# Performance work log

Measured on AMD Instinct MI355X. Metric: run time of the kernel, lower is better.

The kernel has to match this reference:

```python
import jax, jax.numpy as jnp
import numpy as np

N_EMBD = 512
N_HEAD = 8
HEAD_DIM = N_EMBD // N_HEAD


def setup_inputs() -> dict:
    key = jax.random.key(0)
    ks = jax.random.split(key, 10)
    B, Tx, Tc, C = 8, 1024, 2048, N_EMBD
    s = 1.0 / np.sqrt(C)
    return {
        "x": jax.random.normal(ks[0], (B, Tx, C), dtype=jnp.float32),
        "context": jax.random.normal(ks[1], (B, Tc, C), dtype=jnp.float32),
        "Wq": jax.random.normal(ks[2], (C, C), dtype=jnp.float32) * s,
        "bq": jnp.zeros((C,), dtype=jnp.float32),
        "Wk": jax.random.normal(ks[3], (C, C), dtype=jnp.float32) * s,
        "bk": jnp.zeros((C,), dtype=jnp.float32),
        "Wv": jax.random.normal(ks[4], (C, C), dtype=jnp.float32) * s,
        "bv": jnp.zeros((C,), dtype=jnp.float32),
        "Wo": jax.random.normal(ks[5], (C, C), dtype=jnp.float32) * s,
        "bo": jnp.zeros((C,), dtype=jnp.float32),
    }


def reference(x, context, Wq, bq, Wk, bk, Wv, bv, Wo, bo):
    B, Tx, C = x.shape
    Tc = context.shape[1]
    nh, hd = N_HEAD, C // N_HEAD
    # projections (torch Linear: y = x @ W.T + b)
    q = (x @ Wq.T + bq).reshape(B, Tx, nh, hd).transpose(0, 2, 1, 3)
    k = (context @ Wk.T + bk).reshape(B, Tc, nh, hd).transpose(0, 2, 1, 3)
    v = (context @ Wv.T + bv).reshape(B, Tc, nh, hd).transpose(0, 2, 1, 3)
    # attention scores (B, nh, Tx, Tc)
    att = jnp.einsum("bhqd,bhkd->bhqk", q, k) * (1.0 / np.sqrt(hd))
    att = jax.nn.softmax(att, axis=-1)
    y = jnp.einsum("bhqk,bhkd->bhqd", att, v)
    y = y.transpose(0, 2, 1, 3).reshape(B, Tx, C)
    att_mean = att.mean(axis=1)  # (B, Tx, Tc)
    y = y @ Wo.T + bo
    return (y, att_mean)
```

## Files before the change

kernel.cpp:

```cpp
#include <hip/hip_runtime.h>

#define DEVI __device__ __forceinline__

typedef short bf16x8 __attribute__((ext_vector_type(8)));
typedef short bf16x4 __attribute__((ext_vector_type(4)));
typedef float f32x4 __attribute__((ext_vector_type(4)));

constexpr int Bb = 8, TX = 1024, TC = 2048, CC = 512, NH = 8, HD = 64;
constexpr float LOG2E = 1.44269504f;

DEVI unsigned short f2bf(float f) {
  union { float f; unsigned u; } v; v.f = f;
  return (unsigned short)((v.u + 0x7FFFu + ((v.u >> 16) & 1u)) >> 16);
}

DEVI unsigned cvtpk(float lo, float hi) {
  unsigned r;
  asm("v_cvt_pk_bf16_f32 %0, %1, %2" : "=v"(r) : "v"(lo), "v"(hi));
  return r;
}

DEVI f32x4 mfma16(bf16x8 a, bf16x8 b, f32x4 c) {
  return __builtin_amdgcn_mfma_f32_16x16x32_bf16(a, b, c, 0, 0, 0);
}

DEVI f32x4 zero4() { f32x4 z = {0.f, 0.f, 0.f, 0.f}; return z; }

DEVI float max3f(float a, float b, float c) { return fmaxf(fmaxf(a, b), c); }

DEVI void gload_lds16(const unsigned short* g, unsigned short* l) {
  __builtin_amdgcn_global_load_lds(
      (const __attribute__((address_space(1))) void*)g,
      (__attribute__((address_space(3))) void*)l, 16, 0, 0);
}

__global__ __launch_bounds__(256) void cvt_bf16(
    const float* __restrict__ src, unsigned short* __restrict__ dst, int n8) {
  int i = blockIdx.x * 256 + threadIdx.x;
  const int stride = gridDim.x * 256;
  for (; i < n8; i += stride) {
    f32x4 a = *(const f32x4*)(src + (size_t)i * 8);
    f32x4 b = *(const f32x4*)(src + (size_t)i * 8 + 4);
    bf16x8 v;
#pragma unroll
    for (int j = 0; j < 4; j++) {
      v[j] = (short)f2bf(a[j]);
      v[j + 4] = (short)f2bf(b[j]);
    }
    *(bf16x8*)(dst + (size_t)i * 8) = v;
  }
}

template <int MODE>
__global__ __launch_bounds__(256, 3) void gemm128(
    const unsigned short* __restrict__ A, const unsigned short* __restrict__ W,
    const float* __restrict__ bias, void* __restrict__ outp, int tlog2, float scale) {
  __shared__ __align__(16) unsigned short As[2][128 * 32];
  __shared__ __align__(16) unsigned short Bs[2][128 * 32];

  const int tid = threadIdx.x;
  const int wid = tid >> 6, l = tid & 63, l15 = l & 15, lhi = l >> 4;
  const int wm = wid >> 1, wn = wid & 1;
  const int mbase = blockIdx.y * 128, nbase = blockIdx.x * 128;

  f32x4 acc[4][4];
#pragma unroll
  for (int i = 0; i < 4; i++)
#pragma unroll
    for (int j = 0; j < 4; j++) acc[i][j] = zero4();

  auto stage = [&](int buf, int k0) {
#pragma unroll
    for (int i = 0; i < 2; i++) {
      const int u = wid * 128 + i * 64 + l;
      const int row = u >> 2;
      const int gc = ((u & 3) ^ ((row >> 1) & 3)) * 8;
      const int lo = (wid * 128 + i * 64) * 8;
      gload_lds16(A + (size_t)(mbase + row) * CC + k0 + gc, &As[buf][lo]);
      gload_lds16(W + (size_t)(nbase + row) * CC + k0 + gc, &Bs[buf][lo]);
    }
  };

  stage(0, 0);

  const int sA = (lhi ^ ((l15 >> 1) & 3)) << 3;

  constexpr int NK = CC / 32;
  for (int kt = 0; kt < NK; kt++) {
    const int cur = kt & 1;
    __syncthreads();
    if (kt + 1 < NK) stage(cur ^ 1, (kt + 1) * 32);

    bf16x8 af[4], bfr[4];
#pragma unroll
    for (int mi = 0; mi < 4; mi++)
      af[mi] = *(const bf16x8*)&As[cur][(wm * 64 + mi * 16 + l15) * 32 + sA];
#pragma unroll
    for (int ni = 0; ni < 4; ni++)
      bfr[ni] = *(const bf16x8*)&Bs[cur][(wn * 64 + ni * 16 + l15) * 32 + sA];
#pragma unroll
    for (int mi = 0; mi < 4; mi++)
#pragma unroll
      for (int ni = 0; ni < 4; ni++)
        acc[mi][ni] = mfma16(af[mi], bfr[ni], acc[mi][ni]);
  }

#pragma unroll
  for (int mi = 0; mi < 4; mi++)
#pragma unroll
    for (int ni = 0; ni < 4; ni++)
#pragma unroll
      for (int r = 0; r < 4; r++) {
        int grow = mbase + wm * 64 + mi * 16 + 4 * lhi + r;
        int gcol = nbase + wn * 64 + ni * 16 + l15;
        float val = (acc[mi][ni][r] + bias[gcol]) * scale;
        if (MODE == 0) {
          int T = 1 << tlog2;
          int bq = grow >> tlog2, tt = grow & (T - 1);
          int h = gcol >> 6, d = gcol & 63;
          size_t oidx = ((size_t)(bq * NH + h) * T + tt) * HD + d;
          ((unsigned short*)outp)[oidx] = f2bf(val);
        } else {
          ((float*)outp)[(size_t)grow * CC + gcol] = val;
        }
      }
}

__global__ __launch_bounds__(256, 2) void kv_gemm128(
    const unsigned short* __restrict__ A, const unsigned short* __restrict__ Wk,
    const unsigned short* __restrict__ Wv, const float* __restrict__ bk,
    const float* __restrict__ bv, unsigned short* __restrict__ k_out,
    unsigned short* __restrict__ v_out) {
  __shared__ __align__(16) unsigned short As[2][128 * 32];
  __shared__ __align__(16) unsigned short Bks[2][128 * 32];
  __shared__ __align__(16) unsigned short Bvs[2][128 * 32];

  const int tid = threadIdx.x;
  const int wid = tid >> 6, l = tid & 63, l15 = l & 15, lhi = l >> 4;
  const int wm = wid >> 1, wn = wid & 1;
  const int mbase = blockIdx.y * 128, nbase = blockIdx.x * 128;

  f32x4 acck[4][4], accv[4][4];
#pragma unroll
  for (int i = 0; i < 4; i++)
#pragma unroll
    for (int j = 0; j < 4; j++) { acck[i][j] = zero4(); accv[i][j] = zero4(); }

  auto stage = [&](int buf, int k0) {
#pragma unroll
    for (int i = 0; i < 2; i++) {
      const int u = wid * 128 + i * 64 + l;
      const int row = u >> 2;
      const int gc = ((u & 3) ^ ((row >> 1) & 3)) * 8;
      const int lo = (wid * 128 + i * 64) * 8;
      gload_lds16(A + (size_t)(mbase + row) * CC + k0 + gc, &As[buf][lo]);
      gload_lds16(Wk + (size_t)(nbase + row) * CC + k0 + gc, &Bks[buf][lo]);
      gload_lds16(Wv + (size_t)(nbase + row) * CC + k0 + gc, &Bvs[buf][lo]);
    }
  };

  stage(0, 0);

  const int sA = (lhi ^ ((l15 >> 1) & 3)) << 3;

  constexpr int NK = CC / 32;
  for (int kt = 0; kt < NK; kt++) {
    const int cur = kt & 1;
    __syncthreads();
    if (kt + 1 < NK) stage(cur ^ 1, (kt + 1) * 32);

    bf16x8 af[4], kf[4], vf[4];
#pragma unroll
    for (int mi = 0; mi < 4; mi++)
      af[mi] = *(const bf16x8*)&As[cur][(wm * 64 + mi * 16 + l15) * 32 + sA];
#pragma unroll
    for (int ni = 0; ni < 4; ni++) {
      kf[ni] = *(const bf16x8*)&Bks[cur][(wn * 64 + ni * 16 + l15) * 32 + sA];
      vf[ni] = *(const bf16x8*)&Bvs[cur][(wn * 64 + ni * 16 + l15) * 32 + sA];
    }
#pragma unroll
    for (int mi = 0; mi < 4; mi++)
#pragma unroll
      for (int ni = 0; ni < 4; ni++) {
        acck[mi][ni] = mfma16(af[mi], kf[ni], acck[mi][ni]);
        accv[mi][ni] = mfma16(af[mi], vf[ni], accv[mi][ni]);
      }
  }

#pragma unroll
  for (int mi = 0; mi < 4; mi++)
#pragma unroll
    for (int ni = 0; ni < 4; ni++)
#pragma unroll
      for (int r = 0; r < 4; r++) {
        int grow = mbase + wm * 64 + mi * 16 + 4 * lhi + r;
        int gcol = nbase + wn * 64 + ni * 16 + l15;
        int bq = grow >> 11, tt = grow & (TC - 1);
        int h = gcol >> 6, d = gcol & 63;
        float kv = acck[mi][ni][r] + bk[gcol];
        float vv = accv[mi][ni][r] + bv[gcol];
        k_out[((size_t)(bq * NH + h) * TC + tt) * HD + d] = f2bf(kv);
        v_out[((size_t)(bq * NH + h) * HD + d) * TC + tt] = f2bf(vv);
      }
}

__global__ __launch_bounds__(512) void attn_fwd(
    const unsigned short* __restrict__ Qw, const unsigned short* __restrict__ Kw,
    const unsigned short* __restrict__ Vtw, unsigned short* __restrict__ y_pre,
    float* __restrict__ m_ws, float* __restrict__ il_ws) {
  __shared__ __align__(16) unsigned short ktl[2][64 * 64];
  __shared__ __align__(16) unsigned short vtl[2][64 * 64];

  const int tid = threadIdx.x;
  const int wid = tid >> 6, l = tid & 63, l15 = l & 15, lhi = l >> 4;
  const int qg = blockIdx.x, h = blockIdx.y, b = blockIdx.z;
  const int qbase = qg * 128 + wid * 16;

  const unsigned short* Qh = Qw + (size_t)(b * NH + h) * TX * HD;
  const unsigned short* Kh = Kw + (size_t)(b * NH + h) * TC * HD;
  const unsigned short* Vt = Vtw + (size_t)(b * NH + h) * TC * HD;

  bf16x8 aq0 = *(const bf16x8*)(Qh + (size_t)(qbase + l15) * HD + lhi * 8);
  bf16x8 aq1 = *(const bf16x8*)(Qh + (size_t)(qbase + l15) * HD + 32 + lhi * 8);

  bf16x8 ones;
#pragma unroll
  for (int j = 0; j < 8; j++) ones[j] = (short)0x3F80;

  f32x4 accy[4];
#pragma unroll
  for (int db = 0; db < 4; db++) accy[db] = zero4();
  f32x4 accl = zero4();
  float mrun = -1e30f;

  const int sl0 = l15 + ((lhi & 1) << 5);
  const int sl1 = sl0 + 16;
  const bool sel = ((lhi >> 1) & 1) != 0;

  const int rs0 = (lhi ^ (l15 & 7)) << 3;
  const int rs1 = ((lhi ^ 4) ^ (l15 & 7)) << 3;

  const int sr = tid >> 3;
  const int ssw = ((tid & 7) ^ (sr & 7)) << 3;
  const int sc0 = (tid & 7) * 8;

  bf16x8 kr = *(const bf16x8*)(Kh + (size_t)sr * HD + sc0);
  bf16x8 vp = *(const bf16x8*)(Vt + (size_t)sr * TC + sc0);
  *(bf16x8*)&ktl[0][sr * 64 + ssw] = kr;
  *(bf16x8*)&vtl[0][sr * 64 + ssw] = vp;
  __syncthreads();

  constexpr int NT = TC / 64;
  for (int kt = 0; kt < NT; kt++) {
    const int cur = kt & 1;

    if (kt + 1 < NT) {
      const int keyn = (kt + 1) * 64;
      kr = *(const bf16x8*)(Kh + (size_t)(keyn + sr) * HD + sc0);
      vp = *(const bf16x8*)(Vt + (size_t)sr * TC + keyn + sc0);
    }

    f32x4 s[4];
    __builtin_amdgcn_s_setprio(1);
#pragma unroll
    for (int kb = 0; kb < 4; kb++) {
      bf16x8 bk0 = *(const bf16x8*)&ktl[cur][(kb * 16 + l15) * 64 + rs0];
      bf16x8 bk1 = *(const bf16x8*)&ktl[cur][(kb * 16 + l15) * 64 + rs1];
      f32x4 a = zero4();
      a = mfma16(bk0, aq0, a);
      a = mfma16(bk1, aq1, a);
      s[kb] = a;
    }
    __builtin_amdgcn_s_setprio(0);

    float t0 = max3f(s[0][0], s[0][1], s[0][2]);
    float t1 = max3f(s[0][3], s[1][0], s[1][1]);
    float t2 = max3f(s[1][2], s[1][3], s[2][0]);
    float t3 = max3f(s[2][1], s[2][2], s[2][3]);
    float t4 = max3f(s[3][0], s[3][1], s[3][2]);
    float mx = fmaxf(max3f(t0, t1, t2), max3f(t3, t4, s[3][3]));
    mx = fmaxf(mx, __shfl_xor(mx, 16));
    mx = fmaxf(mx, __shfl_xor(mx, 32));

    if (__any(mx - mrun > 7.0f)) {
      float mn = fmaxf(mrun, mx);
      float sc = exp2f(mrun - mn);
      mrun = mn;
#pragma unroll
      for (int r = 0; r < 4; r++) accl[r] *= sc;
#pragma unroll
      for (int db = 0; db < 4; db++)
#pragma unroll
        for (int r = 0; r < 4; r++) accy[db][r] *= sc;
    }

    float p[4][4];
#pragma unroll
    for (int kb = 0; kb < 4; kb++)
#pragma unroll
      for (int r = 0; r < 4; r++) p[kb][r] = exp2f(s[kb][r] - mrun);

    unsigned pkw[4][2];
#pragma unroll
    for (int kb = 0; kb < 4; kb++) {
      pkw[kb][0] = cvtpk(p[kb][0], p[kb][1]);
      pkw[kb][1] = cvtpk(p[kb][2], p[kb][3]);
    }
    unsigned a00 = (unsigned)__shfl((int)pkw[0][0], sl0);
    unsigned a01 = (unsigned)__shfl((int)pkw[0][1], sl0);
    unsigned a10 = (unsigned)__shfl((int)pkw[1][0], sl0);
    unsigned a11 = (unsigned)__shfl((int)pkw[1][1], sl0);
    unsigned c00 = (unsigned)__shfl((int)pkw[0][0], sl1);
    unsigned c01 = (unsigned)__shfl((int)pkw[0][1], sl1);
    unsigned c10 = (unsigned)__shfl((int)pkw[1][0], sl1);
    unsigned c11 = (unsigned)__shfl((int)pkw[1][1], sl1);
    unsigned e00 = (unsigned)__shfl((int)pkw[2][0], sl0);
    unsigned e01 = (unsigned)__shfl((int)pkw[2][1], sl0);
    unsigned e10 = (unsigned)__shfl((int)pkw[3][0], sl0);
    unsigned e11 = (unsigned)__shfl((int)pkw[3][1], sl0);
    unsigned g00 = (unsigned)__shfl((int)pkw[2][0], sl1);
    unsigned g01 = (unsigned)__shfl((int)pkw[2][1], sl1);
    unsigned g10 = (unsigned)__shfl((int)pkw[3][0], sl1);
    unsigned g11 = (unsigned)__shfl((int)pkw[3][1], sl1);
    union { unsigned u[4]; bf16x8 v; } B0, B1;
    B0.u[0] = sel ? a10 : a00;
    B0.u[1] = sel ? a11 : a01;
    B0.u[2] = sel ? c10 : c00;
    B0.u[3] = sel ? c11 : c01;
    B1.u[0] = sel ? e10 : e00;
    B1.u[1] = sel ? e11 : e01;
    B1.u[2] = sel ? g10 : g00;
    B1.u[3] = sel ? g11 : g01;

    __builtin_amdgcn_s_setprio(1);
#pragma unroll
    for (int db = 0; db < 4; db++) {
      bf16x8 bv0 = *(const bf16x8*)&vtl[cur][(db * 16 + l15) * 64 + rs0];
      bf16x8 bv1 = *(const bf16x8*)&vtl[cur][(db * 16 + l15) * 64 + rs1];
      accy[db] = mfma16(bv0, B0.v, accy[db]);
      accy[db] = mfma16(bv1, B1.v, accy[db]);
    }
    accl = mfma16(ones, B0.v, accl);
    accl = mfma16(ones, B1.v, accl);
    __builtin_amdgcn_s_setprio(0);

    if (kt + 1 < NT) {
      const int nxt = cur ^ 1;
      *(bf16x8*)&ktl[nxt][sr * 64 + ssw] = kr;
      *(bf16x8*)&vtl[nxt][sr * 64 + ssw] = vp;
    }
    __syncthreads();
  }

  const float il = 1.f / accl[0];

#pragma unroll
  for (int db = 0; db < 4; db++) {
    bf16x4 o;
#pragma unroll
    for (int r = 0; r < 4; r++) o[r] = (short)f2bf(accy[db][r] * il);
    *(bf16x4*)(y_pre + (size_t)(b * TX + qbase + l15) * CC + h * HD + db * 16 +
               4 * lhi) = o;
  }
  if (lhi == 0) {
    int idx = (b * NH + h) * TX + qbase + l15;
    m_ws[idx] = mrun;
    il_ws[idx] = il;
  }
}

__global__ __launch_bounds__(512) void att_mean_k(
    const unsigned short* __restrict__ Qw, const unsigned short* __restrict__ Kw,
    const float* __restrict__ m_ws, const float* __restrict__ il_ws,
    float* __restrict__ attm) {
  __shared__ __align__(16) unsigned short ktl[2][64 * 64];

  const int tid = threadIdx.x;
  const int wid = tid >> 6, l = tid & 63, l15 = l & 15, lhi = l >> 4;
  const int qbase = blockIdx.x * 128 + wid * 16;
  const int keyb = blockIdx.y * 64;
  const int b = blockIdx.z;

  const unsigned short* Qb = Qw + (size_t)b * NH * TX * HD;
  const unsigned short* Kb = Kw + (size_t)b * NH * TC * HD;

  const int rs0 = (lhi ^ (l15 & 7)) << 3;
  const int rs1 = ((lhi ^ 4) ^ (l15 & 7)) << 3;

  const int sr = tid >> 3;
  const int ssw = ((tid & 7) ^ (sr & 7)) << 3;
  const int sc0 = (tid & 7) * 8;

  bf16x8 aq0[2], aq1[2];
  f32x4 mm[2], ii[2];

  auto load_q = [&](int h, int p) {
    const unsigned short* qp =
        Qb + ((size_t)h * TX + qbase + l15) * HD + lhi * 8;
    aq0[p] = *(const bf16x8*)qp;
    aq1[p] = *(const bf16x8*)(qp + 32);
    mm[p] = *(const f32x4*)(m_ws + (size_t)(b * NH + h) * TX + qbase + 4 * lhi);
    ii[p] = *(const f32x4*)(il_ws + (size_t)(b * NH + h) * TX + qbase + 4 * lhi);
  };

  bf16x8 kr = *(const bf16x8*)(Kb + ((size_t)keyb + sr) * HD + sc0);
  load_q(0, 0);
  *(bf16x8*)&ktl[0][sr * 64 + ssw] = kr;
  __syncthreads();

  f32x4 am[4];
#pragma unroll
  for (int kb = 0; kb < 4; kb++) am[kb] = zero4();

#pragma unroll
  for (int h = 0; h < NH; h++) {
    const int cur = h & 1;

    if (h + 1 < NH) {
      kr = *(const bf16x8*)(Kb + ((size_t)(h + 1) * TC + keyb + sr) * HD + sc0);
      load_q(h + 1, cur ^ 1);
    }

#pragma unroll
    for (int kb = 0; kb < 4; kb++) {
      bf16x8 bk0 = *(const bf16x8*)&ktl[cur][(kb * 16 + l15) * 64 + rs0];
      bf16x8 bk1 = *(const bf16x8*)&ktl[cur][(kb * 16 + l15) * 64 + rs1];
      f32x4 a = zero4();
      a = mfma16(aq0[cur], bk0, a);
      a = mfma16(aq1[cur], bk1, a);
#pragma unroll
      for (int r = 0; r < 4; r++)
        am[kb][r] += exp2f(a[r] - mm[cur][r]) * ii[cur][r];
    }

    if (h + 1 < NH) {
      const int nxt = cur ^ 1;
      *(bf16x8*)&ktl[nxt][sr * 64 + ssw] = kr;
    }
    __syncthreads();
  }

#pragma unroll
  for (int kb = 0; kb < 4; kb++)
#pragma unroll
    for (int r = 0; r < 4; r++) {
      int trow = qbase + 4 * lhi + r;
      attm[(size_t)(b * TX + trow) * TC + keyb + kb * 16 + l15] = am[kb][r] * 0.125f;
    }
}

extern "C" void kernel_launch(void* const* d_in, const int* in_sizes, int n_in,
                              void* d_out, int out_size, void* d_ws, size_t ws_size,
                              hipStream_t stream) {
  const float* x   = (const float*)d_in[0];
  const float* ctx = (const float*)d_in[1];
  const float* Wq  = (const float*)d_in[2];
  const float* bq  = (const float*)d_in[3];
  const float* Wk  = (const float*)d_in[4];
  const float* bk  = (const float*)d_in[5];
  const float* Wv  = (const float*)d_in[6];
  const float* bv  = (const float*)d_in[7];
  const float* Wo  = (const float*)d_in[8];
  const float* bo  = (const float*)d_in[9];

  float* y_out = (float*)d_out;
  float* attm  = y_out + (size_t)Bb * TX * CC;

  unsigned short* q_ws = (unsigned short*)d_ws;
  unsigned short* k_ws = q_ws + (size_t)Bb * NH * TX * HD;
  unsigned short* v_ws = k_ws + (size_t)Bb * NH * TC * HD;
  float* m_ws  = (float*)(v_ws + (size_t)Bb * NH * TC * HD);
  float* il_ws = m_ws + (size_t)Bb * NH * TX;
  unsigned short* y_pre = (unsigned short*)(il_ws + (size_t)Bb * NH * TX);
  unsigned short* wb = y_pre + (size_t)Bb * TX * CC;
  unsigned short* wbq = wb, *wbk = wb + CC * CC, *wbv = wb + 2 * CC * CC,
                 *wbo = wb + 3 * CC * CC;

  unsigned short* xb = k_ws;
  unsigned short* cb = (unsigned short*)attm;

  const int NX8 = Bb * TX * CC / 8, NC8 = Bb * TC * CC / 8, NW8 = CC * CC / 8;
  cvt_bf16<<<dim3(2048), 256, 0, stream>>>(x, xb, NX8);
  cvt_bf16<<<dim3(2048), 256, 0, stream>>>(ctx, cb, NC8);
  cvt_bf16<<<dim3(128), 256, 0, stream>>>(Wq, wbq, NW8);
  cvt_bf16<<<dim3(128), 256, 0, stream>>>(Wk, wbk, NW8);
  cvt_bf16<<<dim3(128), 256, 0, stream>>>(Wv, wbv, NW8);
  cvt_bf16<<<dim3(128), 256, 0, stream>>>(Wo, wbo, NW8);

  gemm128<0><<<dim3(CC / 128, (Bb * TX) / 128), 256, 0, stream>>>(
      xb, wbq, bq, q_ws, 10, 0.125f * LOG2E);
  kv_gemm128<<<dim3(CC / 128, (Bb * TC) / 128), 256, 0, stream>>>(
      cb, wbk, wbv, bk, bv, k_ws, v_ws);
  attn_fwd<<<dim3(TX / 128, NH, Bb), 512, 0, stream>>>(q_ws, k_ws, v_ws, y_pre, m_ws, il_ws);
  att_mean_k<<<dim3(TX / 128, TC / 64, Bb), 512, 0, stream>>>(q_ws, k_ws, m_ws, il_ws, attm);
  gemm128<1><<<dim3(CC / 128, (Bb * TX) / 128), 256, 0, stream>>>(
      y_pre, wbo, bo, y_out, 10, 1.0f);
}
```

Measured before the change: 220.7 us.

## Merge conversion kernels and preload all K heads into LDS in att_mean

The six fp32-to-bf16 conversion launches become one grid-stride kernel covering all six tensors, which removes launch gaps. In att_mean_k, all eight heads' K tiles are now loaded up front into LDS with direct global-to-LDS loads, in a single batch followed by one barrier. This replaces the per-head double-buffered register staging and its per-iteration __syncthreads, and Q, m and il prefetch is deepened to three slots. LDS per block grows to 64KB, which can limit how many blocks fit per CU despite the launch_bounds occupancy hint.

```diff
diff --git a/kernel.cpp b/kernel.cpp
--- a/kernel.cpp
+++ b/kernel.cpp
@@ -34,11 +34,9 @@
       (__attribute__((address_space(3))) void*)l, 16, 0, 0);
 }
 
-__global__ __launch_bounds__(256) void cvt_bf16(
-    const float* __restrict__ src, unsigned short* __restrict__ dst, int n8) {
-  int i = blockIdx.x * 256 + threadIdx.x;
-  const int stride = gridDim.x * 256;
-  for (; i < n8; i += stride) {
+DEVI void cvt_region(const float* __restrict__ src,
+                     unsigned short* __restrict__ dst, int n8, int i0, int stride) {
+  for (int i = i0; i < n8; i += stride) {
     f32x4 a = *(const f32x4*)(src + (size_t)i * 8);
     f32x4 b = *(const f32x4*)(src + (size_t)i * 8 + 4);
     bf16x8 v;
@@ -49,6 +47,23 @@
     }
     *(bf16x8*)(dst + (size_t)i * 8) = v;
   }
+}
+
+__global__ __launch_bounds__(256) void cvt_all(
+    const float* __restrict__ s0, unsigned short* __restrict__ d0, int n0,
+    const float* __restrict__ s1, unsigned short* __restrict__ d1, int n1,
+    const float* __restrict__ s2, unsigned short* __restrict__ d2, int n2,
+    const float* __restrict__ s3, unsigned short* __restrict__ d3, int n3,
+    const float* __restrict__ s4, unsigned short* __restrict__ d4, int n4,
+    const float* __restrict__ s5, unsigned short* __restrict__ d5, int n5) {
+  const int i0 = blockIdx.x * 256 + threadIdx.x;
+  const int stride = gridDim.x * 256;
+  cvt_region(s0, d0, n0, i0, stride);
+  cvt_region(s1, d1, n1, i0, stride);
+  cvt_region(s2, d2, n2, i0, stride);
+  cvt_region(s3, d3, n3, i0, stride);
+  cvt_region(s4, d4, n4, i0, stride);
+  cvt_region(s5, d5, n5, i0, stride);
 }
 
 template <int MODE>
@@ -369,11 +384,11 @@
   }
 }
 
-__global__ __launch_bounds__(512) void att_mean_k(
+__global__ __launch_bounds__(512, 4) void att_mean_k(
     const unsigned short* __restrict__ Qw, const unsigned short* __restrict__ Kw,
     const float* __restrict__ m_ws, const float* __restrict__ il_ws,
     float* __restrict__ attm) {
-  __shared__ __align__(16) unsigned short ktl[2][64 * 64];
+  __shared__ __align__(16) unsigned short ktl[NH][64 * 64];
 
   const int tid = threadIdx.x;
   const int wid = tid >> 6, l = tid & 63, l15 = l & 15, lhi = l >> 4;
@@ -387,12 +402,11 @@
   const int rs0 = (lhi ^ (l15 & 7)) << 3;
   const int rs1 = ((lhi ^ 4) ^ (l15 & 7)) << 3;
 
-  const int sr = tid >> 3;
-  const int ssw = ((tid & 7) ^ (sr & 7)) << 3;
-  const int sc0 = (tid & 7) * 8;
-
-  bf16x8 aq0[2], aq1[2];
-  f32x4 mm[2], ii[2];
+  const int srow = (wid * 64 + l) >> 3;
+  const int sgc = ((l & 7) ^ (srow & 7)) * 8;
+
+  bf16x8 aq0[3], aq1[3];
+  f32x4 mm[3], ii[3];
 
   auto load_q = [&](int h, int p) {
     const unsigned short* qp =
@@ -403,9 +417,12 @@
     ii[p] = *(const f32x4*)(il_ws + (size_t)(b * NH + h) * TX + qbase + 4 * lhi);
   };
 
-  bf16x8 kr = *(const bf16x8*)(Kb + ((size_t)keyb + sr) * HD + sc0);
+#pragma unroll
+  for (int h = 0; h < NH; h++)
+    gload_lds16(Kb + ((size_t)h * TC + keyb + srow) * HD + sgc,
+                &ktl[h][wid * 512]);
   load_q(0, 0);
-  *(bf16x8*)&ktl[0][sr * 64 + ssw] = kr;
+  load_q(1, 1);
   __syncthreads();
 
   f32x4 am[4];
@@ -414,30 +431,20 @@
 
 #pragma unroll
   for (int h = 0; h < NH; h++) {
-    const int cur = h & 1;
-
-    if (h + 1 < NH) {
-      kr = *(const bf16x8*)(Kb + ((size_t)(h + 1) * TC + keyb + sr) * HD + sc0);
-      load_q(h + 1, cur ^ 1);
-    }
+    const int p = h % 3;
+    if (h + 2 < NH) load_q(h + 2, (h + 2) % 3);
 
 #pragma unroll
     for (int kb = 0; kb < 4; kb++) {
-      bf16x8 bk0 = *(const bf16x8*)&ktl[cur][(kb * 16 + l15) * 64 + rs0];
-      bf16x8 bk1 = *(const bf16x8*)&ktl[cur][(kb * 16 + l15) * 64 + rs1];
+      bf16x8 bk0 = *(const bf16x8*)&ktl[h][(kb * 16 + l15) * 64 + rs0];
+      bf16x8 bk1 = *(const bf16x8*)&ktl[h][(kb * 16 + l15) * 64 + rs1];
       f32x4 a = zero4();
-      a = mfma16(aq0[cur], bk0, a);
-      a = mfma16(aq1[cur], bk1, a);
+      a = mfma16(aq0[p], bk0, a);
+      a = mfma16(aq1[p], bk1, a);
 #pragma unroll
       for (int r = 0; r < 4; r++)
-        am[kb][r] += exp2f(a[r] - mm[cur][r]) * ii[cur][r];
-    }
-
-    if (h + 1 < NH) {
-      const int nxt = cur ^ 1;
-      *(bf16x8*)&ktl[nxt][sr * 64 + ssw] = kr;
-    }
-    __syncthreads();
+        am[kb][r] += exp2f(a[r] - mm[p][r]) * ii[p][r];
+    }
   }
 
 #pragma unroll
@@ -480,12 +487,9 @@
   unsigned short* cb = (unsigned short*)attm;
 
   const int NX8 = Bb * TX * CC / 8, NC8 = Bb * TC * CC / 8, NW8 = CC * CC / 8;
-  cvt_bf16<<<dim3(2048), 256, 0, stream>>>(x, xb, NX8);
-  cvt_bf16<<<dim3(2048), 256, 0, stream>>>(ctx, cb, NC8);
-  cvt_bf16<<<dim3(128), 256, 0, stream>>>(Wq, wbq, NW8);
-  cvt_bf16<<<dim3(128), 256, 0, stream>>>(Wk, wbk, NW8);
-  cvt_bf16<<<dim3(128), 256, 0, stream>>>(Wv, wbv, NW8);
-  cvt_bf16<<<dim3(128), 256, 0, stream>>>(Wo, wbo, NW8);
+  cvt_all<<<dim3(2048), 256, 0, stream>>>(x, xb, NX8, ctx, cb, NC8,
+                                          Wq, wbq, NW8, Wk, wbk, NW8,
+                                          Wv, wbv, NW8, Wo, wbo, NW8);
 
   gemm128<0><<<dim3(CC / 128, (Bb * TX) / 128), 256, 0, stream>>>(
       xb, wbq, bq, q_ws, 10, 0.125f * LOG2E);
```

New measurement: 285.9 us. +29.5%, slower.
